# Kernel tuning notes

Measured on AMD Instinct MI355X. Metric: run time of the kernel, lower is better.

The kernel has to match this reference:

```python
import jax, jax.numpy as jnp
import numpy as np

B, N, C, H, L, WSZ = 4, 16384, 1024, 16, 256, 512
Dh = C // H
Nb = N // B
NW = Nb // WSZ
EPS = 1e-6
SCALE = Dh ** -0.5


def _ln(h, g=None, b=None):
    m = h.mean(-1, keepdims=True)
    v = h.var(-1, keepdims=True)
    h = (h - m) * jax.lax.rsqrt(v + EPS)
    if g is not None:
        h = h * g + b
    return h


def setup_inputs() -> dict:
    key = jax.random.key(0)
    ks = jax.random.split(key, 16)
    s = 0.02
    return {
        'x': jax.random.normal(ks[0], (N, C), jnp.float32),
        'context': jax.random.normal(ks[1], (B, L, C), jnp.float32),
        'mod': jax.random.normal(ks[2], (B, C), jnp.float32),
        'W_mod': jax.random.normal(ks[3], (C, 6 * C), jnp.float32) * s,
        'b_mod': jnp.zeros((6 * C,), jnp.float32),
        'gamma2': jnp.ones((C,), jnp.float32),
        'beta2': jnp.zeros((C,), jnp.float32),
        'W_qkv': jax.random.normal(ks[4], (C, 3 * C), jnp.float32) * s,
        'b_qkv': jnp.zeros((3 * C,), jnp.float32),
        'W_so': jax.random.normal(ks[5], (C, C), jnp.float32) * s,
        'b_so': jnp.zeros((C,), jnp.float32),
        'W_q': jax.random.normal(ks[6], (C, C), jnp.float32) * s,
        'b_q': jnp.zeros((C,), jnp.float32),
        'W_kv': jax.random.normal(ks[7], (C, 2 * C), jnp.float32) * s,
        'b_kv': jnp.zeros((2 * C,), jnp.float32),
        'W_co': jax.random.normal(ks[8], (C, C), jnp.float32) * s,
        'b_co': jnp.zeros((C,), jnp.float32),
        'W_m1': jax.random.normal(ks[9], (C, 4 * C), jnp.float32) * s,
        'b_m1': jnp.zeros((4 * C,), jnp.float32),
        'W_m2': jax.random.normal(ks[10], (4 * C, C), jnp.float32) * s,
        'b_m2': jnp.zeros((C,), jnp.float32),
    }


def reference(x, context, mod, W_mod, b_mod, gamma2, beta2, W_qkv, b_qkv,
              W_so, b_so, W_q, b_q, W_kv, b_kv, W_co, b_co,
              W_m1, b_m1, W_m2, b_m2):
    xb = x.reshape(B, Nb, C)

    # AdaLN modulation: SiLU -> Linear -> 6 chunks, broadcast per batch item
    m6 = jax.nn.silu(mod) @ W_mod + b_mod                   # [B, 6C]
    sh_msa, sc_msa, g_msa, sh_mlp, sc_mlp, g_mlp = jnp.split(m6, 6, axis=-1)

    # --- windowed sparse self-attention ---
    h = _ln(xb) * (1.0 + sc_msa[:, None]) + sh_msa[:, None]
    qkv = (h @ W_qkv + b_qkv).reshape(B, NW, WSZ, 3, H, Dh)
    q, k, v = qkv[:, :, :, 0], qkv[:, :, :, 1], qkv[:, :, :, 2]
    a = jax.nn.softmax(jnp.einsum('bwqhd,bwkhd->bwhqk', q, k) * SCALE, axis=-1)
    o = jnp.einsum('bwhqk,bwkhd->bwqhd', a, v).reshape(B, Nb, C)
    xb = xb + g_msa[:, None] * (o @ W_so + b_so)

    # --- full cross-attention to per-batch context ---
    h = _ln(xb, gamma2, beta2)
    q = (h @ W_q + b_q).reshape(B, Nb, H, Dh)
    kv = (context @ W_kv + b_kv).reshape(B, L, 2, H, Dh)
    k, v = kv[:, :, 0], kv[:, :, 1]
    a = jax.nn.softmax(jnp.einsum('bqhd,bkhd->bhqk', q, k) * SCALE, axis=-1)
    o = jnp.einsum('bhqk,bkhd->bqhd', a, v).reshape(B, Nb, C)
    xb = xb + (o @ W_co + b_co)

    # --- modulated sparse FFN ---
    h = _ln(xb) * (1.0 + sc_mlp[:, None]) + sh_mlp[:, None]
    h = jax.nn.gelu(h @ W_m1 + b_m1, approximate=True)
    xb = xb + g_mlp[:, None] * (h @ W_m2 + b_m2)

    return xb.reshape(N, C)
```

## Files before the change

kernel.cpp:

```cpp
#include <hip/hip_runtime.h>

typedef unsigned short u16;
typedef __attribute__((ext_vector_type(8))) short short8;
typedef __attribute__((ext_vector_type(4))) float f32x4;

#define SCALE_ 0.125f

struct __align__(8) U16x4 { u16 x, y, z, w; };

__device__ __forceinline__ u16 f2b(float f) {
  union { float f; unsigned u; } c; c.f = f;
  unsigned u = c.u;
  u += 0x7fffu + ((u >> 16) & 1u);
  return (u16)(u >> 16);
}

__device__ __forceinline__ void gload16(const void* g, void* l) {
  __builtin_amdgcn_global_load_lds((const __attribute__((address_space(1))) void*)g,
                                   (__attribute__((address_space(3))) void*)l,
                                   16, 0, 0);
}

__device__ __forceinline__ float gelu_t(float x) {
  float z = 1.5957691216057308f * (x + 0.044715f * x * x * x);
  return x / (1.0f + __expf(-z));
}

__global__ __launch_bounds__(256) void wcast(const float* __restrict__ W,
                                             u16* __restrict__ Wt, int K, int N) {
  __shared__ float t[32][33];
  const int nb = N >> 5;
  const int k0 = (blockIdx.x / nb) << 5;
  const int n0 = (blockIdx.x % nb) << 5;
  const int tx = threadIdx.x & 31;
  const int ty = threadIdx.x >> 5;
#pragma unroll
  for (int r = 0; r < 32; r += 8) t[ty + r][tx] = W[(size_t)(k0 + ty + r) * N + n0 + tx];
  __syncthreads();
#pragma unroll
  for (int r = 0; r < 32; r += 8) Wt[(size_t)(n0 + ty + r) * K + k0 + tx] = f2b(t[tx][ty + r]);
}

__global__ __launch_bounds__(256) void cast_bf(const float* __restrict__ in,
                                               u16* __restrict__ out) {
  const int i = blockIdx.x * 256 + threadIdx.x;
  const float4 v = ((const float4*)in)[i];
  U16x4 o; o.x = f2b(v.x); o.y = f2b(v.y); o.z = f2b(v.z); o.w = f2b(v.w);
  ((U16x4*)out)[i] = o;
}

__global__ __launch_bounds__(256) void mod_gemm(const float* __restrict__ mod,
                                                const float* __restrict__ Wm,
                                                const float* __restrict__ bm,
                                                float* __restrict__ m6) {
  __shared__ float s[4096];
  for (int i = threadIdx.x; i < 4096; i += 256) {
    float x = mod[i];
    s[i] = x / (1.0f + __expf(-x));
  }
  __syncthreads();
  const int j = blockIdx.x * 256 + threadIdx.x;
  float a0 = bm[j], a1 = a0, a2 = a0, a3 = a0;
#pragma unroll 8
  for (int c = 0; c < 1024; c++) {
    float w = Wm[(size_t)c * 6144 + j];
    a0 += s[c] * w;
    a1 += s[1024 + c] * w;
    a2 += s[2048 + c] * w;
    a3 += s[3072 + c] * w;
  }
  m6[j] = a0; m6[6144 + j] = a1; m6[12288 + j] = a2; m6[18432 + j] = a3;
}

__global__ __launch_bounds__(256) void ln_k(const float* __restrict__ x,
                                            u16* __restrict__ out,
                                            const float* __restrict__ g,
                                            const float* __restrict__ bb,
                                            int batch_stride, int add_one) {
  const int row = blockIdx.x;
  const int tid = threadIdx.x;
  const float4 v = ((const float4*)(x + (size_t)row * 1024))[tid];
  float s = v.x + v.y + v.z + v.w;
  float q = v.x * v.x + v.y * v.y + v.z * v.z + v.w * v.w;
#pragma unroll
  for (int m = 1; m < 64; m <<= 1) {
    s += __shfl_xor(s, m, 64);
    q += __shfl_xor(q, m, 64);
  }
  __shared__ float ps[4], pq[4];
  if ((tid & 63) == 0) { ps[tid >> 6] = s; pq[tid >> 6] = q; }
  __syncthreads();
  s = ps[0] + ps[1] + ps[2] + ps[3];
  q = pq[0] + pq[1] + pq[2] + pq[3];
  const float mean = s * (1.0f / 1024.0f);
  const float var = q * (1.0f / 1024.0f) - mean * mean;
  const float rstd = rsqrtf(var + 1e-6f);
  const int batch = row >> 12;
  const float4 gv = ((const float4*)(g + (size_t)batch * batch_stride))[tid];
  const float4 bv = ((const float4*)(bb + (size_t)batch * batch_stride))[tid];
  const float ao = add_one ? 1.0f : 0.0f;
  U16x4 o;
  o.x = f2b((v.x - mean) * rstd * (gv.x + ao) + bv.x);
  o.y = f2b((v.y - mean) * rstd * (gv.y + ao) + bv.y);
  o.z = f2b((v.z - mean) * rstd * (gv.z + ao) + bv.z);
  o.w = f2b((v.w - mean) * rstd * (gv.w + ao) + bv.w);
  ((U16x4*)(out + (size_t)row * 1024))[tid] = o;
}

template <int EPI>
__global__ __launch_bounds__(256) void gemm_bt(const u16* __restrict__ A,
                                               const u16* __restrict__ Bt,
                                               const float* __restrict__ bias,
                                               void* outp, const float* res,
                                               const float* gate, int M, int N,
                                               int K, int gate_stride) {
  __shared__ __align__(16) u16 As[4096];
  __shared__ __align__(16) u16 Bs[4096];
  const int nb = N >> 7;
  const int bm = (blockIdx.x / nb) << 7;
  const int bn = (blockIdx.x % nb) << 7;
  const int tid = threadIdx.x;
  const int lane = tid & 63;
  const int wv = tid >> 6;
  const int wr = (wv >> 1) << 6;
  const int wc = (wv & 1) << 6;
  const int lrow = lane & 15;
  const int lk = lane >> 4;
  const int srow = tid >> 2;
  const int scol = (tid & 3) << 3;
  const u16* gA = A + (size_t)(bm + srow) * K + scol;
  const u16* gB = Bt + (size_t)(bn + srow) * K + scol;
  const size_t rskip = (size_t)64 * K;
  u16* lA = As + wv * 512;
  u16* lB = Bs + wv * 512;
  f32x4 acc[4][4] = {};
  for (int k0 = 0; k0 < K; k0 += 32) {
    gload16(gA + k0, lA);
    gload16(gA + k0 + rskip, lA + 2048);
    gload16(gB + k0, lB);
    gload16(gB + k0 + rskip, lB + 2048);
    __syncthreads();
    short8 a[4], b[4];
#pragma unroll
    for (int m = 0; m < 4; m++)
      a[m] = *(const short8*)(As + (wr + m * 16 + lrow) * 32 + lk * 8);
#pragma unroll
    for (int n = 0; n < 4; n++)
      b[n] = *(const short8*)(Bs + (wc + n * 16 + lrow) * 32 + lk * 8);
#pragma unroll
    for (int m = 0; m < 4; m++)
#pragma unroll
      for (int n = 0; n < 4; n++)
        acc[m][n] = __builtin_amdgcn_mfma_f32_16x16x32_bf16(a[m], b[n], acc[m][n], 0, 0, 0);
    __syncthreads();
  }
#pragma unroll
  for (int m = 0; m < 4; m++) {
    const int row0 = bm + wr + m * 16 + lk * 4;
#pragma unroll
    for (int n = 0; n < 4; n++) {
      const int col = bn + wc + n * 16 + lrow;
      const float bval = bias[col];
#pragma unroll
      for (int j = 0; j < 4; j++) {
        float v = acc[m][n][j] + bval;
        size_t idx = (size_t)(row0 + j) * N + col;
        ((u16*)outp)[idx] = f2b(v);
      }
    }
  }
}

template <int EPI>
__global__ __launch_bounds__(512, 2) void gemm8p(const u16* __restrict__ A,
                                                 const u16* __restrict__ Bt,
                                                 const float* __restrict__ bias,
                                                 void* outp, const float* res,
                                                 const float* gate, int M, int N,
                                                 int K, int gate_stride) {
  extern __shared__ char smem[];
  const int nb = N >> 8;
  const int nwg = (M >> 8) * nb;
  const int cpx = nwg >> 3;
  const int wg = (blockIdx.x & 7) * cpx + (blockIdx.x >> 3);
  const int bm = (wg / nb) << 8;
  const int bn = (wg % nb) << 8;
  const int tid = threadIdx.x;
  const int lane = tid & 63;
  const int w = tid >> 6;
  const int wm = w >> 2;
  const int wn = w & 3;
  const int lrow = lane & 15;
  const int lk = lane >> 4;
  const int u = (lane & 7) ^ (lane >> 3);
  const int r_off = w * 16 + ((lane >> 3) << 1) + (u >> 2);
  const int c_off = (u & 3) << 3;
  const u16* gA = A + (size_t)(bm + r_off) * K + c_off;
  const u16* gB = Bt + (size_t)(bn + r_off) * K + c_off;
  const size_t l_skip = (size_t)128 * K;
  char* sA = smem;
  char* sB = smem + 65536;
  const int dsb = ((lrow >> 1) << 7) + (((((lrow & 1) << 2) + lk) ^ (lrow >> 1)) << 4);
  const int aQ = wm * 8192;
  const int bQ = wn * 4096;

  f32x4 acc[8][4] = {};
  short8 bq[4];
  short8 af[4];

#define SG_A(d, kh, tt)                                                         \
  { gload16(gA + (size_t)(tt) * 64 + (kh) * 32, sA + (d) * 32768 + (kh) * 16384 + w * 1024);            \
    gload16(gA + l_skip + (size_t)(tt) * 64 + (kh) * 32, sA + (d) * 32768 + (kh) * 16384 + (w + 8) * 1024); }
#define SG_B(d, kh, tt)                                                         \
  { gload16(gB + (size_t)(tt) * 64 + (kh) * 32, sB + (d) * 32768 + (kh) * 16384 + w * 1024);            \
    gload16(gB + l_skip + (size_t)(tt) * 64 + (kh) * 32, sB + (d) * 32768 + (kh) * 16384 + (w + 8) * 1024); }
#define RD_A(d, kh, mh)                                                         \
  _Pragma("unroll") for (int m = 0; m < 4; m++)                                 \
    af[m] = *(const short8*)(sA + (d) * 32768 + (kh) * 16384 + aQ + (mh) * 4096 + m * 1024 + dsb);
#define RD_B(d, kh)                                                             \
  _Pragma("unroll") for (int n = 0; n < 4; n++)                                 \
    bq[n] = *(const short8*)(sB + (d) * 32768 + (kh) * 16384 + bQ + n * 1024 + dsb);
#define MM(mh)                                                                  \
  _Pragma("unroll") for (int m = 0; m < 4; m++)                                 \
    _Pragma("unroll") for (int n = 0; n < 4; n++)                               \
      acc[(mh) * 4 + m][n] =                                                    \
          __builtin_amdgcn_mfma_f32_16x16x32_bf16(af[m], bq[n], acc[(mh) * 4 + m][n], 0, 0, 0);
#define SBAR0 __builtin_amdgcn_sched_barrier(0)
#define VM4   asm volatile("s_waitcnt vmcnt(4)" ::: "memory")

  SG_A(0, 0, 0); SG_B(0, 0, 0); SG_A(0, 1, 0); SG_B(0, 1, 0);
  SBAR0;
  VM4;
  __builtin_amdgcn_s_barrier();

  const int nt = K >> 6;
  for (int t = 0; t < nt; ++t) {
    const int d = t & 1;
    const int dn = d ^ 1;
    const int tn = (t + 1 < nt) ? t + 1 : t;
    {
      RD_A(d, 0, 0); RD_B(d, 0);
      SG_A(dn, 0, tn);
      __builtin_amdgcn_s_setprio(1);
      MM(0);
      __builtin_amdgcn_s_setprio(0);
      SBAR0;
    }
    {
      RD_A(d, 0, 1);
      SG_B(dn, 0, tn);
      SBAR0;
      VM4;
      __builtin_amdgcn_s_barrier();
      SBAR0;
      __builtin_amdgcn_s_setprio(1);
      MM(1);
      __builtin_amdgcn_s_setprio(0);
      SBAR0;
    }
    {
      RD_A(d, 1, 0); RD_B(d, 1);
      SG_A(dn, 1, tn);
      __builtin_amdgcn_s_setprio(1);
      MM(0);
      __builtin_amdgcn_s_setprio(0);
      SBAR0;
    }
    {
      RD_A(d, 1, 1);
      SG_B(dn, 1, tn);
      SBAR0;
      VM4;
      __builtin_amdgcn_s_barrier();
      SBAR0;
      __builtin_amdgcn_s_setprio(1);
      MM(1);
      __builtin_amdgcn_s_setprio(0);
      SBAR0;
    }
  }
  asm volatile("s_waitcnt vmcnt(0)" ::: "memory");
#undef SG_A
#undef SG_B
#undef RD_A
#undef RD_B
#undef MM
#undef SBAR0
#undef VM4

  __syncthreads();
  float* eb = (float*)smem + (size_t)w * 1088;
  const float* grow = nullptr;
  if (EPI == 2 && gate) grow = gate + (size_t)(bm >> 12) * gate_stride;
  const int erow = lane >> 4;
  const int ecol = (lane & 15) << 2;
  const int colb = bn + wn * 64 + ecol;
  const float4 bv4 = *(const float4*)(bias + colb);
  float4 gv4 = make_float4(1.0f, 1.0f, 1.0f, 1.0f);
  if (EPI == 2 && grow) gv4 = *(const float4*)(grow + colb);
#pragma unroll
  for (int m = 0; m < 8; m++) {
#pragma unroll
    for (int n = 0; n < 4; n++)
#pragma unroll
      for (int j = 0; j < 4; j++)
        eb[(lk * 4 + j) * 68 + n * 16 + lrow] = acc[m][n][j];
    const int row0 = bm + wm * 128 + m * 16 + erow;
#pragma unroll
    for (int i = 0; i < 4; i++) {
      const int row = row0 + 4 * i;
      float4 v = *(const float4*)(eb + (erow + 4 * i) * 68 + ecol);
      v.x += bv4.x; v.y += bv4.y; v.z += bv4.z; v.w += bv4.w;
      const size_t base = (size_t)row * N + colb;
      if (EPI == 0) {
        U16x4 o; o.x = f2b(v.x); o.y = f2b(v.y); o.z = f2b(v.z); o.w = f2b(v.w);
        *(U16x4*)((u16*)outp + base) = o;
      } else if (EPI == 1) {
        U16x4 o; o.x = f2b(gelu_t(v.x)); o.y = f2b(gelu_t(v.y));
        o.z = f2b(gelu_t(v.z)); o.w = f2b(gelu_t(v.w));
        *(U16x4*)((u16*)outp + base) = o;
      } else {
        const float4 r4 = *(const float4*)(res + base);
        float4 o;
        o.x = r4.x + gv4.x * v.x; o.y = r4.y + gv4.y * v.y;
        o.z = r4.z + gv4.z * v.z; o.w = r4.w + gv4.w * v.w;
        *(float4*)((float*)outp + base) = o;
      }
    }
  }
}

template <int MODE>
__global__ __launch_bounds__(512) void attn_k(const u16* __restrict__ QKV,
                                              const u16* __restrict__ Q2,
                                              const u16* __restrict__ KV2,
                                              u16* __restrict__ O) {
  __shared__ __align__(16) u16 Ks[4096];
  __shared__ __align__(16) u16 Vt[4096];
  __shared__ __align__(16) u16 Ps[16384];
  const int bid = blockIdx.x;
  const int tid = threadIdx.x;
  const int lane = tid & 63;
  const int wv = tid >> 6;
  const int lrow = lane & 15;
  const int lk = lane >> 4;
  const u16 *qp, *kp, *vp;
  int q_row0, q_stride, kv_row0, kv_stride, nkt, ocol;
  if (MODE == 0) {
    const int qt = bid & 1, h = (bid >> 1) & 15, w = (bid >> 5) & 7, b = bid >> 8;
    const int win = (b * 8 + w) * 512;
    q_row0 = win + qt * 256; q_stride = 3072;
    qp = QKV + h * 64;
    kp = QKV + 1024 + h * 64;
    vp = QKV + 2048 + h * 64;
    kv_row0 = win; kv_stride = 3072; nkt = 8;
    ocol = h * 64;
  } else {
    const int qt = bid & 15, h = (bid >> 4) & 15, b = bid >> 8;
    q_row0 = b * 4096 + qt * 256; q_stride = 1024;
    qp = Q2 + h * 64;
    kp = KV2 + h * 64;
    vp = KV2 + 1024 + h * 64;
    kv_row0 = b * 256; kv_stride = 2048; nkt = 4;
    ocol = h * 64;
  }
  const int qr = q_row0 + wv * 32;
  short8 qf[2][2];
#pragma unroll
  for (int m = 0; m < 2; m++)
#pragma unroll
    for (int kk = 0; kk < 2; kk++)
      qf[m][kk] = *(const short8*)(qp + (size_t)(qr + m * 16 + lrow) * q_stride + kk * 32 + lk * 8);
  f32x4 oa[2][4] = {};
  float lst[2][4];
#pragma unroll
  for (int m = 0; m < 2; m++)
#pragma unroll
    for (int j = 0; j < 4; j++) lst[m][j] = 0.0f;

  u16* Pw = Ps + wv * 2048;
  for (int kt = 0; kt < nkt; kt++) {
    const int kvr = kv_row0 + kt * 64;
    {
      const int r = tid >> 3, c = tid & 7;
      gload16(kp + (size_t)(kvr + r) * kv_stride + (((c) ^ (r & 7)) << 3),
              Ks + wv * 512);
    }
    {
      const int krow = tid >> 3, d0 = (tid & 7) << 3;
      short8 vvv = *(const short8*)(vp + (size_t)(kvr + krow) * kv_stride + d0);
#pragma unroll
      for (int i = 0; i < 8; i++) {
        const int ii = (i + (tid & 7)) & 7;
        const int dd = d0 + ii;
        Vt[dd * 64 + (((krow >> 3) ^ (dd & 7)) << 3) + (krow & 7)] = (u16)vvv[ii];
      }
    }
    __syncthreads();
    f32x4 s[2][4] = {};
    __builtin_amdgcn_s_setprio(1);
#pragma unroll
    for (int n = 0; n < 4; n++)
#pragma unroll
      for (int kk = 0; kk < 2; kk++) {
        short8 kb = *(const short8*)(Ks + (n * 16 + lrow) * 64 + (((kk * 4 + lk) ^ (lrow & 7)) << 3));
        s[0][n] = __builtin_amdgcn_mfma_f32_16x16x32_bf16(qf[0][kk], kb, s[0][n], 0, 0, 0);
        s[1][n] = __builtin_amdgcn_mfma_f32_16x16x32_bf16(qf[1][kk], kb, s[1][n], 0, 0, 0);
      }
    __builtin_amdgcn_s_setprio(0);
#pragma unroll
    for (int m = 0; m < 2; m++)
#pragma unroll
      for (int j = 0; j < 4; j++) {
        const float p0 = __expf(s[m][0][j] * SCALE_);
        const float p1 = __expf(s[m][1][j] * SCALE_);
        const float p2 = __expf(s[m][2][j] * SCALE_);
        const float p3 = __expf(s[m][3][j] * SCALE_);
        lst[m][j] += p0 + p1 + p2 + p3;
        const int prow = m * 16 + lk * 4 + j;
        const int base = prow * 64;
        const int r7 = prow & 7;
        const int kl = lrow >> 3, k7 = lrow & 7;
        Pw[base + (((0 + kl) ^ r7) << 3) + k7] = f2b(p0);
        Pw[base + (((2 + kl) ^ r7) << 3) + k7] = f2b(p1);
        Pw[base + (((4 + kl) ^ r7) << 3) + k7] = f2b(p2);
        Pw[base + (((6 + kl) ^ r7) << 3) + k7] = f2b(p3);
      }
#pragma unroll
    for (int kk = 0; kk < 2; kk++) {
      const int sw = ((kk * 4 + lk) ^ (lrow & 7)) << 3;
      short8 pa0 = *(const short8*)(Pw + lrow * 64 + sw);
      short8 pa1 = *(const short8*)(Pw + (16 + lrow) * 64 + sw);
      __builtin_amdgcn_s_setprio(1);
#pragma unroll
      for (int dn = 0; dn < 4; dn++) {
        short8 vb = *(const short8*)(Vt + (dn * 16 + lrow) * 64 + sw);
        oa[0][dn] = __builtin_amdgcn_mfma_f32_16x16x32_bf16(pa0, vb, oa[0][dn], 0, 0, 0);
        oa[1][dn] = __builtin_amdgcn_mfma_f32_16x16x32_bf16(pa1, vb, oa[1][dn], 0, 0, 0);
      }
      __builtin_amdgcn_s_setprio(0);
    }
    __syncthreads();
  }
#pragma unroll
  for (int m = 0; m < 2; m++)
#pragma unroll
    for (int j = 0; j < 4; j++) {
      float rs = lst[m][j];
      rs += __shfl_xor(rs, 1, 64);
      rs += __shfl_xor(rs, 2, 64);
      rs += __shfl_xor(rs, 4, 64);
      rs += __shfl_xor(rs, 8, 64);
      const float inv = 1.0f / rs;
      const int orow = qr + m * 16 + lk * 4 + j;
#pragma unroll
      for (int dn = 0; dn < 4; dn++)
        O[(size_t)orow * 1024 + ocol + dn * 16 + lrow] = f2b(oa[m][dn][j] * inv);
    }
}

extern "C" void kernel_launch(void* const* d_in, const int* in_sizes, int n_in,
                              void* d_out, int out_size, void* d_ws, size_t ws_size,
                              hipStream_t stream) {
  (void)in_sizes; (void)n_in; (void)out_size; (void)ws_size;
  const float* x      = (const float*)d_in[0];
  const float* ctx    = (const float*)d_in[1];
  const float* mod    = (const float*)d_in[2];
  const float* W_mod  = (const float*)d_in[3];
  const float* b_mod  = (const float*)d_in[4];
  const float* gamma2 = (const float*)d_in[5];
  const float* beta2  = (const float*)d_in[6];
  const float* W_qkv  = (const float*)d_in[7];
  const float* b_qkv  = (const float*)d_in[8];
  const float* W_so   = (const float*)d_in[9];
  const float* b_so   = (const float*)d_in[10];
  const float* W_q    = (const float*)d_in[11];
  const float* b_q    = (const float*)d_in[12];
  const float* W_kv   = (const float*)d_in[13];
  const float* b_kv   = (const float*)d_in[14];
  const float* W_co   = (const float*)d_in[15];
  const float* b_co   = (const float*)d_in[16];
  const float* W_m1   = (const float*)d_in[17];
  const float* b_m1   = (const float*)d_in[18];
  const float* W_m2   = (const float*)d_in[19];
  const float* b_m2   = (const float*)d_in[20];

  char* ws = (char*)d_ws;
  u16*   wt_qkv = (u16*)(ws + 0);
  u16*   wt_so  = (u16*)(ws + 6291456);
  u16*   wt_q   = (u16*)(ws + 8388608);
  u16*   wt_kv  = (u16*)(ws + 10485760);
  u16*   wt_co  = (u16*)(ws + 14680064);
  u16*   wt_m1  = (u16*)(ws + 16777216);
  u16*   wt_m2  = (u16*)(ws + 25165824);
  float* m6     = (float*)(ws + 33554432);
  u16*   ctxb   = (u16*)(ws + 33652736);
  u16*   kvb    = (u16*)(ws + 35749888);
  u16*   bufH   = (u16*)(ws + 39944192);
  u16*   bufO   = (u16*)(ws + 73498624);
  u16*   bufA   = (u16*)(ws + 107053056);
  float* xb1    = (float*)(ws + 107053056 + 50331648);
  float* outp   = (float*)d_out;

  hipFuncSetAttribute(reinterpret_cast<const void*>(&gemm8p<0>),
                      hipFuncAttributeMaxDynamicSharedMemorySize, 131072);
  hipFuncSetAttribute(reinterpret_cast<const void*>(&gemm8p<1>),
                      hipFuncAttributeMaxDynamicSharedMemorySize, 131072);
  hipFuncSetAttribute(reinterpret_cast<const void*>(&gemm8p<2>),
                      hipFuncAttributeMaxDynamicSharedMemorySize, 131072);

  wcast<<<3072, 256, 0, stream>>>(W_qkv, wt_qkv, 1024, 3072);
  wcast<<<1024, 256, 0, stream>>>(W_so,  wt_so,  1024, 1024);
  wcast<<<1024, 256, 0, stream>>>(W_q,   wt_q,   1024, 1024);
  wcast<<<2048, 256, 0, stream>>>(W_kv,  wt_kv,  1024, 2048);
  wcast<<<1024, 256, 0, stream>>>(W_co,  wt_co,  1024, 1024);
  wcast<<<4096, 256, 0, stream>>>(W_m1,  wt_m1,  1024, 4096);
  wcast<<<4096, 256, 0, stream>>>(W_m2,  wt_m2,  4096, 1024);
  cast_bf<<<1024, 256, 0, stream>>>(ctx, ctxb);

  mod_gemm<<<24, 256, 0, stream>>>(mod, W_mod, b_mod, m6);

  ln_k<<<16384, 256, 0, stream>>>(x, bufH, m6 + 1024, m6 + 0, 6144, 1);
  gemm8p<0><<<768, 512, 131072, stream>>>(bufH, wt_qkv, b_qkv, bufA, nullptr, nullptr, 16384, 3072, 1024, 0);
  attn_k<0><<<1024, 512, 0, stream>>>(bufA, nullptr, nullptr, bufO);
  gemm8p<2><<<256, 512, 131072, stream>>>(bufO, wt_so, b_so, xb1, x, m6 + 2048, 16384, 1024, 1024, 6144);

  ln_k<<<16384, 256, 0, stream>>>(xb1, bufH, gamma2, beta2, 0, 0);
  gemm8p<0><<<256, 512, 131072, stream>>>(bufH, wt_q, b_q, bufA, nullptr, nullptr, 16384, 1024, 1024, 0);
  gemm_bt<0><<<128, 256, 0, stream>>>(ctxb, wt_kv, b_kv, kvb, nullptr, nullptr, 1024, 2048, 1024, 0);
  attn_k<1><<<1024, 512, 0, stream>>>(nullptr, bufA, kvb, bufO);
  gemm8p<2><<<256, 512, 131072, stream>>>(bufO, wt_co, b_co, outp, xb1, nullptr, 16384, 1024, 1024, 0);

  ln_k<<<16384, 256, 0, stream>>>(outp, bufH, m6 + 4096, m6 + 3072, 6144, 1);
  gemm8p<1><<<1024, 512, 131072, stream>>>(bufH, wt_m1, b_m1, bufA, nullptr, nullptr, 16384, 4096, 1024, 0);
  gemm8p<2><<<256, 512, 131072, stream>>>(bufA, wt_m2, b_m2, outp, outp, m6 + 5120, 16384, 1024, 4096, 6144);
}
```

Measured before the change: 910.8 us.

## Double-buffer K/V tiles in attention and merge weight-cast launches

The attention kernel now double-buffers the K and transposed V tiles in shared memory. It prefetches the next tile while the current one is used in the MFMA work, which removes one barrier per tile and hides global load latency. The seven weight-transpose casts and the context cast are also merged into a single kernel launch driven by a descriptor table, cutting per-launch overhead. The cost is higher LDS use in attention, which may lower occupancy, plus a small per-block table lookup in the cast kernel.

```diff
diff --git a/kernel.cpp b/kernel.cpp
--- a/kernel.cpp
+++ b/kernel.cpp
@@ -26,12 +26,33 @@
   return x / (1.0f + __expf(-z));
 }
 
-__global__ __launch_bounds__(256) void wcast(const float* __restrict__ W,
-                                             u16* __restrict__ Wt, int K, int N) {
+struct WcastDesc {
+  const float* src[8];
+  void* dst[8];
+  int K[8];
+  int N[8];
+  int ofs[9];
+};
+
+__global__ __launch_bounds__(256) void wcast_all(WcastDesc d) {
   __shared__ float t[32][33];
+  const int bid = blockIdx.x;
+  int i = 0;
+  while (bid >= d.ofs[i + 1]) ++i;
+  const int rb = bid - d.ofs[i];
+  if (d.K[i] == 0) {
+    const int idx = rb * 256 + threadIdx.x;
+    const float4 v = ((const float4*)d.src[i])[idx];
+    U16x4 o; o.x = f2b(v.x); o.y = f2b(v.y); o.z = f2b(v.z); o.w = f2b(v.w);
+    ((U16x4*)d.dst[i])[idx] = o;
+    return;
+  }
+  const float* W = d.src[i];
+  u16* Wt = (u16*)d.dst[i];
+  const int K = d.K[i], N = d.N[i];
   const int nb = N >> 5;
-  const int k0 = (blockIdx.x / nb) << 5;
-  const int n0 = (blockIdx.x % nb) << 5;
+  const int k0 = (rb / nb) << 5;
+  const int n0 = (rb % nb) << 5;
   const int tx = threadIdx.x & 31;
   const int ty = threadIdx.x >> 5;
 #pragma unroll
@@ -39,14 +60,6 @@
   __syncthreads();
 #pragma unroll
   for (int r = 0; r < 32; r += 8) Wt[(size_t)(n0 + ty + r) * K + k0 + tx] = f2b(t[tx][ty + r]);
-}
-
-__global__ __launch_bounds__(256) void cast_bf(const float* __restrict__ in,
-                                               u16* __restrict__ out) {
-  const int i = blockIdx.x * 256 + threadIdx.x;
-  const float4 v = ((const float4*)in)[i];
-  U16x4 o; o.x = f2b(v.x); o.y = f2b(v.y); o.z = f2b(v.z); o.w = f2b(v.w);
-  ((U16x4*)out)[i] = o;
 }
 
 __global__ __launch_bounds__(256) void mod_gemm(const float* __restrict__ mod,
@@ -335,8 +348,8 @@
                                               const u16* __restrict__ Q2,
                                               const u16* __restrict__ KV2,
                                               u16* __restrict__ O) {
-  __shared__ __align__(16) u16 Ks[4096];
-  __shared__ __align__(16) u16 Vt[4096];
+  __shared__ __align__(16) u16 Ks[2][4096];
+  __shared__ __align__(16) u16 Vt[2][4096];
   __shared__ __align__(16) u16 Ps[16384];
   const int bid = blockIdx.x;
   const int tid = threadIdx.x;
@@ -378,36 +391,51 @@
 #pragma unroll
     for (int j = 0; j < 4; j++) lst[m][j] = 0.0f;
 
+  const int srow = tid >> 3;
+  const int schk = tid & 7;
+  {
+    gload16(kp + (size_t)(kv_row0 + srow) * kv_stride + ((schk ^ (srow & 7)) << 3),
+            Ks[0] + wv * 512);
+    short8 vv = *(const short8*)(vp + (size_t)(kv_row0 + srow) * kv_stride + (schk << 3));
+#pragma unroll
+    for (int i = 0; i < 8; i++) {
+      const int ii = (i + schk) & 7;
+      const int dd = (schk << 3) + ii;
+      Vt[0][dd * 64 + (((srow >> 3) ^ (dd & 7)) << 3) + (srow & 7)] = (u16)vv[ii];
+    }
+  }
+  __syncthreads();
+
   u16* Pw = Ps + wv * 2048;
   for (int kt = 0; kt < nkt; kt++) {
-    const int kvr = kv_row0 + kt * 64;
-    {
-      const int r = tid >> 3, c = tid & 7;
-      gload16(kp + (size_t)(kvr + r) * kv_stride + (((c) ^ (r & 7)) << 3),
-              Ks + wv * 512);
-    }
-    {
-      const int krow = tid >> 3, d0 = (tid & 7) << 3;
-      short8 vvv = *(const short8*)(vp + (size_t)(kvr + krow) * kv_stride + d0);
-#pragma unroll
-      for (int i = 0; i < 8; i++) {
-        const int ii = (i + (tid & 7)) & 7;
-        const int dd = d0 + ii;
-        Vt[dd * 64 + (((krow >> 3) ^ (dd & 7)) << 3) + (krow & 7)] = (u16)vvv[ii];
-      }
-    }
-    __syncthreads();
+    const int cur = kt & 1, nxt = cur ^ 1;
+    const int have = (kt + 1 < nkt);
+    short8 vv;
+    if (have) {
+      const int kvr1 = kv_row0 + (kt + 1) * 64;
+      gload16(kp + (size_t)(kvr1 + srow) * kv_stride + ((schk ^ (srow & 7)) << 3),
+              Ks[nxt] + wv * 512);
+      vv = *(const short8*)(vp + (size_t)(kvr1 + srow) * kv_stride + (schk << 3));
+    }
     f32x4 s[2][4] = {};
     __builtin_amdgcn_s_setprio(1);
 #pragma unroll
     for (int n = 0; n < 4; n++)
 #pragma unroll
       for (int kk = 0; kk < 2; kk++) {
-        short8 kb = *(const short8*)(Ks + (n * 16 + lrow) * 64 + (((kk * 4 + lk) ^ (lrow & 7)) << 3));
+        short8 kb = *(const short8*)(Ks[cur] + (n * 16 + lrow) * 64 + (((kk * 4 + lk) ^ (lrow & 7)) << 3));
         s[0][n] = __builtin_amdgcn_mfma_f32_16x16x32_bf16(qf[0][kk], kb, s[0][n], 0, 0, 0);
         s[1][n] = __builtin_amdgcn_mfma_f32_16x16x32_bf16(qf[1][kk], kb, s[1][n], 0, 0, 0);
       }
     __builtin_amdgcn_s_setprio(0);
+    if (have) {
+#pragma unroll
+      for (int i = 0; i < 8; i++) {
+        const int ii = (i + schk) & 7;
+        const int dd = (schk << 3) + ii;
+        Vt[nxt][dd * 64 + (((srow >> 3) ^ (dd & 7)) << 3) + (srow & 7)] = (u16)vv[ii];
+      }
+    }
 #pragma unroll
     for (int m = 0; m < 2; m++)
 #pragma unroll
@@ -434,7 +462,7 @@
       __builtin_amdgcn_s_setprio(1);
 #pragma unroll
       for (int dn = 0; dn < 4; dn++) {
-        short8 vb = *(const short8*)(Vt + (dn * 16 + lrow) * 64 + sw);
+        short8 vb = *(const short8*)(Vt[cur] + (dn * 16 + lrow) * 64 + sw);
         oa[0][dn] = __builtin_amdgcn_mfma_f32_16x16x32_bf16(pa0, vb, oa[0][dn], 0, 0, 0);
         oa[1][dn] = __builtin_amdgcn_mfma_f32_16x16x32_bf16(pa1, vb, oa[1][dn], 0, 0, 0);
       }
@@ -509,14 +537,19 @@
   hipFuncSetAttribute(reinterpret_cast<const void*>(&gemm8p<2>),
                       hipFuncAttributeMaxDynamicSharedMemorySize, 131072);
 
-  wcast<<<3072, 256, 0, stream>>>(W_qkv, wt_qkv, 1024, 3072);
-  wcast<<<1024, 256, 0, stream>>>(W_so,  wt_so,  1024, 1024);
-  wcast<<<1024, 256, 0, stream>>>(W_q,   wt_q,   1024, 1024);
-  wcast<<<2048, 256, 0, stream>>>(W_kv,  wt_kv,  1024, 2048);
-  wcast<<<1024, 256, 0, stream>>>(W_co,  wt_co,  1024, 1024);
-  wcast<<<4096, 256, 0, stream>>>(W_m1,  wt_m1,  1024, 4096);
-  wcast<<<4096, 256, 0, stream>>>(W_m2,  wt_m2,  4096, 1024);
-  cast_bf<<<1024, 256, 0, stream>>>(ctx, ctxb);
+  WcastDesc wd;
+  wd.src[0] = W_qkv; wd.dst[0] = wt_qkv; wd.K[0] = 1024; wd.N[0] = 3072;
+  wd.src[1] = W_so;  wd.dst[1] = wt_so;  wd.K[1] = 1024; wd.N[1] = 1024;
+  wd.src[2] = W_q;   wd.dst[2] = wt_q;   wd.K[2] = 1024; wd.N[2] = 1024;
+  wd.src[3] = W_kv;  wd.dst[3] = wt_kv;  wd.K[3] = 1024; wd.N[3] = 2048;
+  wd.src[4] = W_co;  wd.dst[4] = wt_co;  wd.K[4] = 1024; wd.N[4] = 1024;
+  wd.src[5] = W_m1;  wd.dst[5] = wt_m1;  wd.K[5] = 1024; wd.N[5] = 4096;
+  wd.src[6] = W_m2;  wd.dst[6] = wt_m2;  wd.K[6] = 4096; wd.N[6] = 1024;
+  wd.src[7] = ctx;   wd.dst[7] = ctxb;   wd.K[7] = 0;    wd.N[7] = 0;
+  wd.ofs[0] = 0;     wd.ofs[1] = 3072;  wd.ofs[2] = 4096; wd.ofs[3] = 5120;
+  wd.ofs[4] = 7168;  wd.ofs[5] = 8192;  wd.ofs[6] = 12288; wd.ofs[7] = 16384;
+  wd.ofs[8] = 17408;
+  wcast_all<<<17408, 256, 0, stream>>>(wd);
 
   mod_gemm<<<24, 256, 0, stream>>>(mod, W_mod, b_mod, m6);
 
```

New measurement: 896.2 us. About the same (-1.6%).
